# Optimization experiments

Hardware: AMD Instinct MI355X
Metric: run time of the kernel (lower is better)

Reference implementation:

```python
import jax, jax.numpy as jnp
import numpy as np

IN_CH, OUT_CH, KS = 64, 128, 3
GRID, DEG = 8, 3
STRIDE, PAD = 1, 1
SIZE = IN_CH * KS * KS            # 576
NCOEF = GRID + DEG                # 11
GRID_RANGE = (-1.0, 1.0)


def _xavier_uniform(key, shape):
    fan_out, fan_in = shape
    a = float(np.sqrt(6.0 / (fan_in + fan_out)))
    return jax.random.uniform(key, shape, minval=-a, maxval=a, dtype=jnp.float32)


def setup_inputs() -> dict:
    key = jax.random.key(0)
    k1, k2, k3 = jax.random.split(key, 3)
    x = jax.random.normal(k1, (8, IN_CH, 32, 32), dtype=jnp.float32)
    # non-trainable knot grid, one row per unfolded feature
    knots = jnp.tile(jnp.linspace(GRID_RANGE[0], GRID_RANGE[1], GRID + 1, dtype=jnp.float32)[None, :], (SIZE, 1))
    coeff = 0.1 * jax.random.normal(k2, (OUT_CH, SIZE, NCOEF), dtype=jnp.float32)
    base_weights = _xavier_uniform(k3, (OUT_CH, SIZE))
    spline_weights = jnp.ones((OUT_CH, SIZE), dtype=jnp.float32)
    return {"x": x, "knots": knots, "coeff": coeff,
            "base_weights": base_weights, "spline_weights": spline_weights}


def bspline_basis(x, grid, k):
    # x: (S, P) evaluation points; grid: (S, G+1) knots. Returns (S, G+k, P).
    h = (grid[:, -1:] - grid[:, :1]) / (grid.shape[1] - 1)
    left = grid[:, :1] - h * jnp.arange(k, 0, -1, dtype=x.dtype)
    right = grid[:, -1:] + h * jnp.arange(1, k + 1, dtype=x.dtype)
    g = jnp.concatenate([left, grid, right], axis=1)  # (S, G+1+2k)
    xe = x[:, None, :]
    B = ((xe >= g[:, :-1, None]) & (xe < g[:, 1:, None])).astype(x.dtype)
    for d in range(1, k + 1):  # de Boor recursion over fixed degree
        B = ((xe - g[:, :-(d + 1), None]) / (g[:, d:-1, None] - g[:, :-(d + 1), None]) * B[:, :-1]
             + (g[:, d + 1:, None] - xe) / (g[:, d + 1:, None] - g[:, 1:-d, None]) * B[:, 1:])
    return B


def _unfold(x):
    # torch F.unfold with channel-major (c, kh, kw) feature ordering
    N, C, H, W = x.shape
    xp = jnp.pad(x, ((0, 0), (0, 0), (PAD, PAD), (PAD, PAD)))
    Hp = (H + 2 * PAD - KS) // STRIDE + 1
    Wp = (W + 2 * PAD - KS) // STRIDE + 1
    patches = jnp.stack([xp[:, :, i:i + STRIDE * Hp:STRIDE, j:j + STRIDE * Wp:STRIDE]
                         for i in range(KS) for j in range(KS)], axis=2)  # (N, C, KS*KS, Hp, Wp)
    L = Hp * Wp
    u = patches.reshape(N, SIZE, L)              # (N, size, L)
    u = jnp.transpose(u, (1, 0, 2)).reshape(SIZE, N * L)  # (size, N*L), col = n*L + l
    return u, Hp, Wp


def reference(x, knots, coeff, base_weights, spline_weights):
    N = x.shape[0]
    u, Hp, Wp = _unfold(x)                                   # (size, P)
    base = base_weights @ jax.nn.silu(u)                     # (Cout, P)
    B = bspline_basis(u, knots, DEG)                         # (size, ncoef, P)
    eff = spline_weights[:, :, None] * coeff                 # (Cout, size, ncoef)
    spl = jnp.einsum('csj,sjp->cp', eff, B)                  # (Cout, P)
    out = (base + spl).reshape(OUT_CH, N, Hp, Wp)
    return jnp.transpose(out, (1, 0, 2, 3))                  # (N, Cout, Hp, Wp)
```

## Files before the change

kernel.cpp:

```cpp
#include <hip/hip_runtime.h>


typedef __attribute__((ext_vector_type(8))) short bf16x8;
typedef __attribute__((ext_vector_type(4))) float f32x4;
typedef __attribute__((ext_vector_type(16))) float f32x16;
typedef __attribute__((ext_vector_type(4))) unsigned short u16x4;

#define WSWZ_BYTES 1769472
#define PART_OFF   WSWZ_BYTES

__device__ __forceinline__ short f2bf(float f) {
    union { float f; unsigned u; } c; c.f = f;
    unsigned r = c.u + 0x7fffu + ((c.u >> 16) & 1u);
    return (short)(r >> 16);
}
__device__ __forceinline__ float bf2f(unsigned short u) {
    union { unsigned u; float f; } c; c.u = ((unsigned)u) << 16;
    return c.f;
}

__global__ void kan_weights(const float* __restrict__ coeff,
                            const float* __restrict__ basew,
                            const float* __restrict__ splw,
                            short* __restrict__ Wswz) {
    __shared__ float coeffL[6336];
    __shared__ float basewL[576];
    __shared__ float splwL[576];
    const int co = blockIdx.x;
    const int t  = threadIdx.x;
    const float* crow = coeff + co * 6336;
    for (int i = t; i < 6336; i += 256) coeffL[i] = crow[i];
    for (int i = t; i < 576; i += 256) {
        basewL[i] = basew[co * 576 + i];
        splwL[i]  = splw[co * 576 + i];
    }
    __syncthreads();
    const int cb = co >> 5, lm = co & 31;
    for (int c = t; c < 864; c += 256) {
        int kk16 = c >> 1, kh = c & 1;
        int f  = kk16 / 36;
        int rm = kk16 - f * 36;
        int tap = rm >> 2, q = rm & 3;
        bf16x8 pack;
#pragma unroll
        for (int j = 0; j < 8; ++j) {
            int ci = q * 16 + kh * 8 + j;
            int s  = ci * 9 + tap;
            float v = (f == 0) ? basewL[s] : splwL[s] * coeffL[s * 11 + (f - 1)];
            pack[j] = f2bf(v);
        }
        *(bf16x8*)(Wswz + (size_t)((kk16 * 4 + cb) * 64 + kh * 32 + lm) * 8) = pack;
    }
}

__global__ __launch_bounds__(256, 2)
void kan_gemm(const float* __restrict__ x,
              const short* __restrict__ Wswz,
              float* __restrict__ part) {
    __shared__ unsigned short xs[4 * 64 * 36];
    __shared__ short Bs[3 * 8704];

    const int t  = threadIdx.x;
    const int w  = t >> 6;
    const int l  = t & 63;
    const int ln = l & 31;
    const int kh = l >> 5;

    const int bz    = blockIdx.x;
    const int fg    = bz & 3;
    const int ptile = bz >> 2;
    const int n     = ptile >> 4;
    const int y0    = (ptile & 15) << 1;

#pragma unroll
    for (int it = 0; it < 8; ++it) {
        int cg = t + it * 256;
        int rr = cg >> 9, ci = (cg >> 3) & 63, q = cg & 7;
        int y  = y0 - 1 + rr;
        f32x4 v = {0.f, 0.f, 0.f, 0.f};
        if (y >= 0 && y < 32)
            v = *(const f32x4*)(x + (((n * 64 + ci) * 32 + y) * 32 + q * 4));
        u16x4 p;
        p.x = (unsigned short)f2bf(v.x); p.y = (unsigned short)f2bf(v.y);
        p.z = (unsigned short)f2bf(v.z); p.w = (unsigned short)f2bf(v.w);
        *(u16x4*)&xs[(rr * 64 + ci) * 36 + q * 4] = p;
    }
    __syncthreads();

    const int f0 = fg * 3;
    for (int it = t; it < 1088; it += 256) {
        int rr  = it / 272;
        int rem = it - rr * 272;
        int xp = rem >> 3, cch = rem & 7, c0 = cch << 3;
        bool interior = (xp >= 1 && xp <= 32);
        bf16x8 packs[3];
#pragma unroll
        for (int j = 0; j < 8; ++j) {
            float v = interior ? bf2f(xs[(rr * 64 + c0 + j) * 36 + (xp - 1)]) : 0.f;
            float silu = v / (1.f + __expf(-v));
            float tt = 4.f * v + 7.f;
            int   i0 = -100;
            float b0 = 0.f, b1 = 0.f, b2 = 0.f, b3 = 0.f;
            if (tt >= 0.f && tt < 14.f) {
                i0 = (int)tt;
                float fr  = tt - (float)i0;
                float omf = 1.f - fr;
                float fr2 = fr * fr, fr3 = fr2 * fr;
                b0 = omf * omf * omf * (1.f / 6.f);
                b1 = (3.f * fr3 - 6.f * fr2 + 4.f) * (1.f / 6.f);
                b2 = (-3.f * fr3 + 3.f * fr2 + 3.f * fr + 1.f) * (1.f / 6.f);
                b3 = fr3 * (1.f / 6.f);
            }
#pragma unroll
            for (int p = 0; p < 3; ++p) {
                int f = f0 + p;
                float val;
                if (f == 0) val = silu;
                else {
                    int jj = f - 1;
                    val = 0.f;
                    val = (jj == i0 - 3) ? b0 : val;
                    val = (jj == i0 - 2) ? b1 : val;
                    val = (jj == i0 - 1) ? b2 : val;
                    val = (jj == i0    ) ? b3 : val;
                }
                packs[p][j] = f2bf(val);
            }
        }
        int pix = rr * 34 + xp;
        int swz = (cch ^ (pix & 7)) << 3;
#pragma unroll
        for (int p = 0; p < 3; ++p)
            *(bf16x8*)&Bs[p * 8704 + pix * 64 + swz] = packs[p];
    }
    __syncthreads();

    f32x16 acc[2];
#pragma unroll
    for (int pb = 0; pb < 2; ++pb)
#pragma unroll
        for (int r = 0; r < 16; ++r)
            acc[pb][r] = 0.f;

    const short* Abase = Wswz + (size_t)w * 512 + (size_t)l * 8;
#pragma unroll 1
    for (int p = 0; p < 3; ++p) {
        const short* B0 = Bs + p * 8704;
        const int kbase = (f0 + p) * 36;
#pragma unroll
        for (int rm = 0; rm < 36; ++rm) {
            const int tap = rm >> 2, q = rm & 3;
            const int dy  = tap / 3;
            const int dx  = tap - dy * 3;
            bf16x8 a = *(const bf16x8*)(Abase + (size_t)(kbase + rm) * 2048);
            const int c = q * 2 + kh;
#pragma unroll
            for (int pb = 0; pb < 2; ++pb) {
                int pix = (pb + dy) * 34 + ln + dx;
                bf16x8 b = *(const bf16x8*)&B0[pix * 64 + ((c ^ (pix & 7)) << 3)];
                acc[pb] = __builtin_amdgcn_mfma_f32_32x32x16_bf16(a, b, acc[pb], 0, 0, 0);
            }
        }
    }

    float* dst = part + (size_t)fg * 1048576;
#pragma unroll
    for (int pb = 0; pb < 2; ++pb) {
        int y = y0 + pb;
#pragma unroll
        for (int r = 0; r < 16; ++r) {
            int row = (r & 3) + 8 * (r >> 2) + 4 * kh;
            int co  = w * 32 + row;
            dst[((size_t)(n * 128 + co) * 32 + y) * 32 + ln] = acc[pb][r];
        }
    }
}

__global__ void kan_reduce(const float* __restrict__ part,
                           float* __restrict__ out) {
    int g = blockIdx.x * 256 + threadIdx.x;
    f32x4 a = ((const f32x4*)part)[g];
#pragma unroll
    for (int s = 1; s < 4; ++s)
        a += ((const f32x4*)(part + (size_t)s * 1048576))[g];
    ((f32x4*)out)[g] = a;
}

extern "C" void kernel_launch(void* const* d_in, const int* in_sizes, int n_in,
                              void* d_out, int out_size, void* d_ws, size_t ws_size,
                              hipStream_t stream) {
    const float* x     = (const float*)d_in[0];
    const float* coeff = (const float*)d_in[2];
    const float* basew = (const float*)d_in[3];
    const float* splw  = (const float*)d_in[4];
    float* out = (float*)d_out;

    short* Wswz = (short*)d_ws;
    float* part = (float*)((char*)d_ws + PART_OFF);

    kan_weights<<<128, 256, 0, stream>>>(coeff, basew, splw, Wswz);
    kan_gemm<<<512, 256, 0, stream>>>(x, Wswz, part);
    kan_reduce<<<1024, 256, 0, stream>>>(part, out);
}
```

Before: 107.4 us.

## Split K six ways with atomic accumulation and drop the reduce kernel

The GEMM reduction dimension is now split into 6 groups of 2 feature blocks instead of 4 groups of 3, giving 768 blocks. Each block atomically adds its partial result straight into the output, which the weight-prep kernel now zeroes. This removes the partial buffer and the separate reduce kernel. Smaller LDS (2 B buffers, an x row stride of 34) allows raising launch bounds to 3 blocks per CU, and SiLU is computed only by the group that needs it. The risks are atomic contention on each output element, nondeterministic summation order, and 8-byte LDS stores that may be misaligned with the new 34-element stride.

```diff
diff --git a/kernel.cpp b/kernel.cpp
--- a/kernel.cpp
+++ b/kernel.cpp
@@ -5,9 +5,6 @@
 typedef __attribute__((ext_vector_type(4))) float f32x4;
 typedef __attribute__((ext_vector_type(16))) float f32x16;
 typedef __attribute__((ext_vector_type(4))) unsigned short u16x4;
-
-#define WSWZ_BYTES 1769472
-#define PART_OFF   WSWZ_BYTES
 
 __device__ __forceinline__ short f2bf(float f) {
     union { float f; unsigned u; } c; c.f = f;
@@ -22,12 +19,19 @@
 __global__ void kan_weights(const float* __restrict__ coeff,
                             const float* __restrict__ basew,
                             const float* __restrict__ splw,
-                            short* __restrict__ Wswz) {
+                            short* __restrict__ Wswz,
+                            float* __restrict__ outz) {
     __shared__ float coeffL[6336];
     __shared__ float basewL[576];
     __shared__ float splwL[576];
     const int co = blockIdx.x;
     const int t  = threadIdx.x;
+
+    f32x4 zz = {0.f, 0.f, 0.f, 0.f};
+#pragma unroll
+    for (int i = 0; i < 8; ++i)
+        ((f32x4*)outz)[(size_t)co * 2048 + i * 256 + t] = zz;
+
     const float* crow = coeff + co * 6336;
     for (int i = t; i < 6336; i += 256) coeffL[i] = crow[i];
     for (int i = t; i < 576; i += 256) {
@@ -53,12 +57,12 @@
     }
 }
 
-__global__ __launch_bounds__(256, 2)
+__global__ __launch_bounds__(256, 3)
 void kan_gemm(const float* __restrict__ x,
               const short* __restrict__ Wswz,
-              float* __restrict__ part) {
-    __shared__ unsigned short xs[4 * 64 * 36];
-    __shared__ short Bs[3 * 8704];
+              float* __restrict__ out) {
+    __shared__ unsigned short xs[4 * 64 * 34];
+    __shared__ short Bs[2 * 8704];
 
     const int t  = threadIdx.x;
     const int w  = t >> 6;
@@ -67,8 +71,8 @@
     const int kh = l >> 5;
 
     const int bz    = blockIdx.x;
-    const int fg    = bz & 3;
-    const int ptile = bz >> 2;
+    const int ptile = bz / 6;
+    const int fg    = bz - ptile * 6;
     const int n     = ptile >> 4;
     const int y0    = (ptile & 15) << 1;
 
@@ -83,21 +87,20 @@
         u16x4 p;
         p.x = (unsigned short)f2bf(v.x); p.y = (unsigned short)f2bf(v.y);
         p.z = (unsigned short)f2bf(v.z); p.w = (unsigned short)f2bf(v.w);
-        *(u16x4*)&xs[(rr * 64 + ci) * 36 + q * 4] = p;
+        *(u16x4*)&xs[(rr * 64 + ci) * 34 + q * 4] = p;
     }
     __syncthreads();
 
-    const int f0 = fg * 3;
+    const int f0 = fg * 2;
     for (int it = t; it < 1088; it += 256) {
         int rr  = it / 272;
         int rem = it - rr * 272;
         int xp = rem >> 3, cch = rem & 7, c0 = cch << 3;
         bool interior = (xp >= 1 && xp <= 32);
-        bf16x8 packs[3];
+        bf16x8 packs[2];
 #pragma unroll
         for (int j = 0; j < 8; ++j) {
-            float v = interior ? bf2f(xs[(rr * 64 + c0 + j) * 36 + (xp - 1)]) : 0.f;
-            float silu = v / (1.f + __expf(-v));
+            float v = interior ? bf2f(xs[(rr * 64 + c0 + j) * 34 + (xp - 1)]) : 0.f;
             float tt = 4.f * v + 7.f;
             int   i0 = -100;
             float b0 = 0.f, b1 = 0.f, b2 = 0.f, b3 = 0.f;
@@ -111,8 +114,11 @@
                 b2 = (-3.f * fr3 + 3.f * fr2 + 3.f * fr + 1.f) * (1.f / 6.f);
                 b3 = fr3 * (1.f / 6.f);
             }
+            float silu = 0.f;
+            if (f0 == 0)
+                silu = v * __builtin_amdgcn_rcpf(1.f + __expf(-v));
 #pragma unroll
-            for (int p = 0; p < 3; ++p) {
+            for (int p = 0; p < 2; ++p) {
                 int f = f0 + p;
                 float val;
                 if (f == 0) val = silu;
@@ -130,7 +136,7 @@
         int pix = rr * 34 + xp;
         int swz = (cch ^ (pix & 7)) << 3;
 #pragma unroll
-        for (int p = 0; p < 3; ++p)
+        for (int p = 0; p < 2; ++p)
             *(bf16x8*)&Bs[p * 8704 + pix * 64 + swz] = packs[p];
     }
     __syncthreads();
@@ -144,7 +150,7 @@
 
     const short* Abase = Wswz + (size_t)w * 512 + (size_t)l * 8;
 #pragma unroll 1
-    for (int p = 0; p < 3; ++p) {
+    for (int p = 0; p < 2; ++p) {
         const short* B0 = Bs + p * 8704;
         const int kbase = (f0 + p) * 36;
 #pragma unroll
@@ -163,7 +169,6 @@
         }
     }
 
-    float* dst = part + (size_t)fg * 1048576;
 #pragma unroll
     for (int pb = 0; pb < 2; ++pb) {
         int y = y0 + pb;
@@ -171,19 +176,9 @@
         for (int r = 0; r < 16; ++r) {
             int row = (r & 3) + 8 * (r >> 2) + 4 * kh;
             int co  = w * 32 + row;
-            dst[((size_t)(n * 128 + co) * 32 + y) * 32 + ln] = acc[pb][r];
+            atomicAdd(&out[((size_t)(n * 128 + co) * 32 + y) * 32 + ln], acc[pb][r]);
         }
     }
-}
-
-__global__ void kan_reduce(const float* __restrict__ part,
-                           float* __restrict__ out) {
-    int g = blockIdx.x * 256 + threadIdx.x;
-    f32x4 a = ((const f32x4*)part)[g];
-#pragma unroll
-    for (int s = 1; s < 4; ++s)
-        a += ((const f32x4*)(part + (size_t)s * 1048576))[g];
-    ((f32x4*)out)[g] = a;
 }
 
 extern "C" void kernel_launch(void* const* d_in, const int* in_sizes, int n_in,
@@ -196,9 +191,7 @@
     float* out = (float*)d_out;
 
     short* Wswz = (short*)d_ws;
-    float* part = (float*)((char*)d_ws + PART_OFF);
 
-    kan_weights<<<128, 256, 0, stream>>>(coeff, basew, splw, Wswz);
-    kan_gemm<<<512, 256, 0, stream>>>(x, Wswz, part);
-    kan_reduce<<<1024, 256, 0, stream>>>(part, out);
+    kan_weights<<<128, 256, 0, stream>>>(coeff, basew, splw, Wswz, out);
+    kan_gemm<<<768, 256, 0, stream>>>(x, Wswz, out);
 }
```

After: 119.2 us. 1.11x slower.
